# Optimization experiments

Hardware: AMD Instinct MI355X
Metric: run time of the kernel (lower is better)

Reference implementation:

```python
import jax, jax.numpy as jnp
import numpy as np
import math

B, S, D, H, DFF, NB = 16, 512, 512, 8, 2048, 2
DK = D // H
L = 3 * NB  # NB blocks_1 layers + 2*NB blocks_2 layers
NEG = -1e32
LN_EPS = 1e-5


def _layernorm(x, g, b):
    mu = jnp.mean(x, -1, keepdims=True)
    var = jnp.mean((x - mu) ** 2, -1, keepdims=True)
    return (x - mu) * jax.lax.rsqrt(var + LN_EPS) * g + b


def _attention(q, k, v, mask, gamma, zero_pad):
    # q,k,v: [B,H,S,DK]; mask: [S,S] bool; gamma: [H]
    scores = jnp.einsum('bhid,bhjd->bhij', q, k) / math.sqrt(DK)
    maskf = mask.astype(scores.dtype)
    # no-grad distance-decay block (torch.no_grad + .detach())
    p = jax.nn.softmax(jnp.where(mask, scores, NEG), axis=-1) * maskf
    distcum = jnp.cumsum(p, axis=-1)
    disttot = jnp.sum(p, axis=-1, keepdims=True)
    idx = jnp.arange(S, dtype=scores.dtype)
    pos = jnp.abs(idx[None, :] - idx[:, None])  # |i-j|, [S,S]
    dist = jnp.sqrt(jnp.clip((disttot - distcum) * pos, 0.0, None))
    dist = jax.lax.stop_gradient(dist)
    g = -jax.nn.softplus(gamma)[None, :, None, None]  # [1,H,1,1]
    total_effect = jnp.clip(jnp.exp(dist * g), 1e-5, 1e5)
    scores = jnp.where(mask, scores * total_effect, NEG)
    attn = jax.nn.softmax(scores, axis=-1)
    if zero_pad:
        attn = attn.at[:, :, 0, :].set(0.0)
    return jnp.einsum('bhij,bhjd->bhid', attn, v)


def _mha(q, k, v, mask, zero_pad, Wk, bk, Wv, bv, Wo, bo, gam):
    # kq_same=True: queries also use the k projection
    def proj(x, W, b):
        return (x @ W + b).reshape(B, S, H, DK).transpose(0, 2, 1, 3)
    qh = proj(q, Wk, bk)
    kh = proj(k, Wk, bk)
    vh = proj(v, Wv, bv)
    out = _attention(qh, kh, vh, mask, gam, zero_pad)
    out = out.transpose(0, 2, 1, 3).reshape(B, S, D)
    return out @ Wo + bo


def _layer(mask_flag, query, key_, values, apply_pos, p):
    (Wk, bk, Wv, bv, Wo, bo, gam, g1, bn1, W1, bf1, W2, bf2, g2, bn2) = p
    idx = jnp.arange(S)
    if mask_flag == 1:
        mask = idx[None, :] <= idx[:, None]  # peek current + past
    else:
        mask = idx[None, :] < idx[:, None]   # strictly past
    zero_pad = (mask_flag == 0)
    q2 = _mha(query, key_, values, mask, zero_pad, Wk, bk, Wv, bv, Wo, bo, gam)
    query = _layernorm(query + q2, g1, bn1)
    if apply_pos:
        q2 = jax.nn.relu(query @ W1 + bf1) @ W2 + bf2
        query = _layernorm(query + q2, g2, bn2)
    return query


def _forward(q_embed_data, qa_embed_data, pid_embed_data, params):
    # emb_type='qid' (no 'pdiff') -> pid_embed_data unused inside attention
    def pslice(l):
        return tuple(a[l] for a in params)
    y = qa_embed_data
    x = q_embed_data
    for l in range(NB):  # blocks_1: self-attn on y, mask=1
        y = _layer(1, y, y, y, True, pslice(l))
    for i in range(NB):  # blocks_2: alternating (mask=1, no FFN) / (mask=0, values=y)
        x = _layer(1, x, x, x, False, pslice(NB + 2 * i))
        x = _layer(0, x, x, y, True, pslice(NB + 2 * i + 1))
    return x, y


def setup_inputs() -> dict:
    key = jax.random.key(0)
    ks = jax.random.split(key, 10)
    sD = 1.0 / math.sqrt(D)
    sF = 1.0 / math.sqrt(DFF)
    f32 = jnp.float32
    return {
        'q_embed_data': jax.random.normal(ks[0], (B, S, D), f32),
        'qa_embed_data': jax.random.normal(ks[1], (B, S, D), f32),
        'pid_embed_data': jax.random.normal(ks[2], (B, S, D), f32),
        'Wk': jax.random.normal(ks[3], (L, D, D), f32) * sD,
        'bk': jnp.zeros((L, D), f32),
        'Wv': jax.random.normal(ks[4], (L, D, D), f32) * sD,
        'bv': jnp.zeros((L, D), f32),
        'Wo': jax.random.normal(ks[5], (L, D, D), f32) * sD,
        'bo': jnp.zeros((L, D), f32),
        'gammas': jax.random.normal(ks[6], (L, H), f32) * 0.5,
        'ln1_g': jnp.ones((L, D), f32),
        'ln1_b': jnp.zeros((L, D), f32),
        'W1': jax.random.normal(ks[7], (L, D, DFF), f32) * sD,
        'b1': jnp.zeros((L, DFF), f32),
        'W2': jax.random.normal(ks[8], (L, DFF, D), f32) * sF,
        'b2': jnp.zeros((L, D), f32),
        'ln2_g': jnp.ones((L, D), f32),
        'ln2_b': jnp.zeros((L, D), f32),
    }


def reference(q_embed_data, qa_embed_data, pid_embed_data, Wk, bk, Wv, bv, Wo, bo,
              gammas, ln1_g, ln1_b, W1, b1, W2, b2, ln2_g, ln2_b):
    params = (Wk, bk, Wv, bv, Wo, bo, gammas, ln1_g, ln1_b, W1, b1, W2, b2, ln2_g, ln2_b)
    x, y = _forward(q_embed_data, qa_embed_data, pid_embed_data, params)
    return (x, y)
```

## Files before the change

kernel.cpp:

```cpp
#include <hip/hip_runtime.h>
#include <hip/hip_bf16.h>

#define Bsz  16
#define Sl   512
#define Dm   512
#define Hn   8
#define DKh  64
#define DFFn 2048
#define MROWS (Bsz * Sl)
#define NEGV (-1e32f)

typedef _Float16 f16;
typedef f16 f16x8 __attribute__((ext_vector_type(8)));
typedef f16 f16x4 __attribute__((ext_vector_type(4)));
typedef float f32x4 __attribute__((ext_vector_type(4)));

#define GLDS16(g, l) __builtin_amdgcn_global_load_lds( \
    (const __attribute__((address_space(1))) void*)(g), \
    (__attribute__((address_space(3))) void*)(l), 16, 0, 0)

__global__ void k_copy2(const float* __restrict__ in, float* __restrict__ out,
                        f16* __restrict__ outh, int n) {
    int i = blockIdx.x * 256 + threadIdx.x;
    if (i < n) { float v = in[i]; out[i] = v; outh[i] = (f16)v; }
}

__global__ __launch_bounds__(256) void k_wconv(const float* __restrict__ src,
        f16* __restrict__ dst, int K, int N, int lmap)
{
    __shared__ float T[32][36];
    int z = blockIdx.z;
    int ls = lmap ? (z < 2 ? z : 2 * z - 1) : z;
    const float* S = src + (size_t)ls * K * N;
    f16* Dt = dst + (size_t)z * K * N;
    int n0 = blockIdx.x * 32, k0 = blockIdx.y * 32;
    int t = threadIdx.x;
    int r = t >> 3, c = (t & 7) * 4;
    float4 v = *(const float4*)(S + (size_t)(k0 + r) * N + n0 + c);
    T[r][c] = v.x; T[r][c + 1] = v.y; T[r][c + 2] = v.z; T[r][c + 3] = v.w;
    __syncthreads();
    int n = t >> 3, kq = (t & 7) * 4;
    f16x4 o = { (f16)T[kq][n], (f16)T[kq + 1][n], (f16)T[kq + 2][n], (f16)T[kq + 3][n] };
    *(f16x4*)(Dt + (size_t)(n0 + n) * K + k0 + kq) = o;
}

template <int RELU, int OUT16, int VTOUT, int BK64>
__global__ __launch_bounds__(256) void k_gemm(
    const f16* __restrict__ A, const f16* __restrict__ Bt,
    const float* __restrict__ bias, float* __restrict__ C, f16* __restrict__ Ch,
    int M, int N, int K)
{
    constexpr int HL = BK64 ? 2 : 1;
    constexpr int BUF = HL * 4096;
    __shared__ f16 As[2 * BUF];
    __shared__ f16 Bs[2 * BUF];
    int tid = threadIdx.x;
    int w = tid >> 6, lane = tid & 63;
    int ln = lane & 15, rg = lane >> 4;
    int wr = w >> 1, wc = w & 1;
    int m0 = blockIdx.y * 128, n0 = blockIdx.x * 128;

    int s0 = tid, s1 = 256 + tid;
    int r0s = s0 >> 2, c0s = ((s0 & 3) ^ ((s0 >> 3) & 3));
    int r1s = s1 >> 2, c1s = ((s1 & 3) ^ ((s1 >> 3) & 3));

    const f16* a0 = A + (size_t)(m0 + r0s) * K + c0s * 8;
    const f16* a1 = A + (size_t)(m0 + r1s) * K + c1s * 8;
    const f16* b0 = Bt + (size_t)(n0 + r0s) * K + c0s * 8;
    const f16* b1 = Bt + (size_t)(n0 + r1s) * K + c1s * 8;

    int cc8 = (rg ^ ((ln >> 1) & 3)) * 8;

    f32x4 acc[4][4] = {};

    int nk = K >> (BK64 ? 6 : 5);

    auto STAGE = [&](int nb, int kt) {
        f16* lA = As + nb * BUF + w * 512;
        f16* lB = Bs + nb * BUF + w * 512;
        GLDS16(a0 + kt, lA);
        GLDS16(a1 + kt, lA + 2048);
        GLDS16(b0 + kt, lB);
        GLDS16(b1 + kt, lB + 2048);
        if (BK64) {
            GLDS16(a0 + kt + 32, lA + 4096);
            GLDS16(a1 + kt + 32, lA + 4096 + 2048);
            GLDS16(b0 + kt + 32, lB + 4096);
            GLDS16(b1 + kt + 32, lB + 4096 + 2048);
        }
    };

    STAGE(0, 0);
    __syncthreads();

    int cur = 0;
    for (int t = 0; t < nk; ++t) {
        if (t + 1 < nk) STAGE(cur ^ 1, (t + 1) << (BK64 ? 6 : 5));

#pragma unroll
        for (int hh = 0; hh < HL; ++hh) {
            const f16* Ab = As + cur * BUF + hh * 4096;
            const f16* Bb = Bs + cur * BUF + hh * 4096;
            f16x8 af[4], bf[4];
#pragma unroll
            for (int i = 0; i < 4; ++i) {
                int m = wr * 64 + i * 16 + ln;
                af[i] = *(const f16x8*)(Ab + m * 32 + cc8);
                int nn = wc * 64 + i * 16 + ln;
                bf[i] = *(const f16x8*)(Bb + nn * 32 + cc8);
            }
#pragma unroll
            for (int i = 0; i < 4; ++i)
#pragma unroll
                for (int j = 0; j < 4; ++j)
                    acc[i][j] = __builtin_amdgcn_mfma_f32_16x16x32_f16(af[i], bf[j], acc[i][j], 0, 0, 0);
        }

        __syncthreads();
        cur ^= 1;
    }

#pragma unroll
    for (int j = 0; j < 4; ++j) {
        int col = n0 + wc * 64 + j * 16 + ln;
        float bj = bias[col];
#pragma unroll
        for (int i = 0; i < 4; ++i) {
            int rb = m0 + wr * 64 + i * 16 + rg * 4;
            if (VTOUT) {
                int bq = rb >> 9, s = rb & 511;
                int hh = col >> 6, dk = col & 63;
                f16x4 o;
#pragma unroll
                for (int r = 0; r < 4; ++r) o[r] = (f16)(acc[i][j][r] + bj);
                *(f16x4*)(Ch + (((size_t)(bq * 8 + hh) * 64 + dk) << 9) + s) = o;
            } else {
#pragma unroll
                for (int r = 0; r < 4; ++r) {
                    float v = acc[i][j][r] + bj;
                    if (RELU) v = fmaxf(v, 0.f);
                    if (OUT16) Ch[(size_t)(rb + r) * N + col] = (f16)v;
                    else       C [(size_t)(rb + r) * N + col] = v;
                }
            }
        }
    }
}

__global__ __launch_bounds__(256, 4) void k_attn(
    const f16* __restrict__ Qh, const f16* __restrict__ VT,
    f16* __restrict__ O, const float* __restrict__ gam, int maskflag)
{
    __shared__ float Sc[16][516];
    f16* Ph = (f16*)Sc;

    int tid = threadIdx.x;
    int w = tid >> 6, lane = tid & 63;
    int ln = lane & 15, rg = lane >> 4;

    int bid = blockIdx.x;
    int lbid = (bid & 7) * 512 + (bid >> 3);
    int tile = 31 - (lbid & 31);
    int bh = lbid >> 5;
    int b = bh >> 3, h = bh & 7;
    int i0 = tile * 16;
    int jtc = (tile >> 2) + 1;
    int units = jtc * 4;

    const f16* Qbase = Qh + ((size_t)b * Sl) * Dm + h * DKh;

    float gm = gam[h];
    float g = -((gm > 20.f) ? gm : log1pf(__expf(gm)));

    f16x8 aq0 = *(const f16x8*)(Qbase + (size_t)(i0 + ln) * Dm + rg * 8);
    f16x8 aq1 = *(const f16x8*)(Qbase + (size_t)(i0 + ln) * Dm + 32 + rg * 8);

    for (int u = w; u < units; u += 4) {
        const f16* kb = Qbase + (size_t)(u * 16 + ln) * Dm + rg * 8;
        f16x8 b0 = *(const f16x8*)(kb);
        f16x8 b1 = *(const f16x8*)(kb + 32);
        f32x4 c = {};
        c = __builtin_amdgcn_mfma_f32_16x16x32_f16(aq0, b0, c, 0, 0, 0);
        c = __builtin_amdgcn_mfma_f32_16x16x32_f16(aq1, b1, c, 0, 0, 0);
#pragma unroll
        for (int r = 0; r < 4; ++r)
            Sc[rg * 4 + r][u * 16 + ln] = c[r];
    }
    __syncthreads();

    int jbase = lane * jtc;
    float st[4][8];
    if ((jtc & 3) == 0) {
#pragma unroll
        for (int q = 0; q < 4; ++q) {
            int r = w * 4 + q;
            float4 t0 = *(float4*)&Sc[r][jbase];
            st[q][0] = t0.x; st[q][1] = t0.y; st[q][2] = t0.z; st[q][3] = t0.w;
            if (jtc == 8) {
                float4 t1 = *(float4*)&Sc[r][jbase + 4];
                st[q][4] = t1.x; st[q][5] = t1.y; st[q][6] = t1.z; st[q][7] = t1.w;
            }
        }
    } else {
#pragma unroll
        for (int q = 0; q < 4; ++q) {
            int r = w * 4 + q;
#pragma unroll
            for (int k = 0; k < 8; ++k)
                if (k < jtc) st[q][k] = Sc[r][jbase + k];
        }
    }
    __syncthreads();

    int im = i0 + w * 4;
    float cs[4][8], run[4], sl[4];
#pragma unroll
    for (int q = 0; q < 4; ++q) {
        int jmax = maskflag ? (im + q) : (im + q - 1);
        run[q] = 0.f;
#pragma unroll
        for (int k = 0; k < 8; ++k) if (k < jtc) {
            int j = jbase + k;
            float s = (j <= jmax) ? st[q][k] * 0.125f : NEGV;
            st[q][k] = s;
            run[q] += __expf(s);
            cs[q][k] = run[q];
        }
        sl[q] = run[q];
    }
#pragma unroll
    for (int off = 1; off < 64; off <<= 1) {
        float n0 = __shfl_up(sl[0], off);
        float n1 = __shfl_up(sl[1], off);
        float n2 = __shfl_up(sl[2], off);
        float n3 = __shfl_up(sl[3], off);
        if (lane >= off) { sl[0] += n0; sl[1] += n1; sl[2] += n2; sl[3] += n3; }
    }
    float Z2[4];
#pragma unroll
    for (int q = 0; q < 4; ++q) {
        float excl = sl[q] - run[q];
        float Z = __shfl(sl[q], 63);
        float inv = 1.f / Z;
        int i = im + q;
        int jmax = maskflag ? i : (i - 1);
        float z2 = 0.f;
#pragma unroll
        for (int k = 0; k < 8; ++k) if (k < jtc) {
            int j = jbase + k;
            float rem = (Z - excl - cs[q][k]) * inv;
            float pos = fabsf((float)(i - j));
            float dd = fmaxf(rem * pos, 0.f);
            float te = __expf(sqrtf(dd) * g);
            te = fminf(fmaxf(te, 1e-5f), 1e5f);
            float sc = (j <= jmax) ? st[q][k] * te : NEGV;
            float pe = __expf(sc);
            st[q][k] = pe;
            z2 += pe;
        }
        Z2[q] = z2;
    }
#pragma unroll
    for (int off = 32; off >= 1; off >>= 1) {
        Z2[0] += __shfl_xor(Z2[0], off);
        Z2[1] += __shfl_xor(Z2[1], off);
        Z2[2] += __shfl_xor(Z2[2], off);
        Z2[3] += __shfl_xor(Z2[3], off);
    }
#pragma unroll
    for (int q = 0; q < 4; ++q) {
        int r = w * 4 + q;
        int i = im + q;
        float inv2 = 1.f / Z2[q];
        int zp = (maskflag == 0) && (i == 0);
        if (jtc == 8) {
            int slot = (lane & ~7) | ((lane & 7) ^ (r & 7));
            f16x8 o8;
#pragma unroll
            for (int k = 0; k < 8; ++k)
                o8[k] = (f16)(zp ? 0.f : st[q][k] * inv2);
            *(f16x8*)(Ph + r * 512 + slot * 8) = o8;
        } else {
#pragma unroll
            for (int k = 0; k < 8; ++k) if (k < jtc) {
                int j = jbase + k;
                int cj = j >> 3;
                int slot = (cj & ~7) | ((cj & 7) ^ (r & 7));
                float a = zp ? 0.f : st[q][k] * inv2;
                Ph[r * 512 + slot * 8 + (j & 7)] = (f16)a;
            }
        }
    }
    __syncthreads();

    const f16* vbase = VT + ((size_t)bh * 64 + w * 16 + ln) * 512 + rg * 8;
    f32x4 oa0 = {}, oa1 = {};
#pragma unroll
    for (int f = 0; f < 16; ++f) if (f < 2 * jtc) {
        f16x8 bv = *(const f16x8*)(vbase + (f >> 1) * 64 + (f & 1) * 32);
        int c = (f >> 1) * 8 + (f & 1) * 4 + rg;
        int slot = (c & ~7) | ((c & 7) ^ (ln & 7));
        f16x8 ap = *(const f16x8*)(Ph + ln * 512 + slot * 8);
        if (f & 1) oa1 = __builtin_amdgcn_mfma_f32_16x16x32_f16(ap, bv, oa1, 0, 0, 0);
        else       oa0 = __builtin_amdgcn_mfma_f32_16x16x32_f16(ap, bv, oa0, 0, 0, 0);
    }
    f32x4 oa = oa0 + oa1;

    f16* ob = O + ((size_t)b * Sl + i0 + rg * 4) * Dm + h * DKh + w * 16 + ln;
#pragma unroll
    for (int r = 0; r < 4; ++r)
        ob[(size_t)r * Dm] = (f16)oa[r];
}

__global__ __launch_bounds__(256) void k_ln(
    const float* __restrict__ Xn, const float* __restrict__ Rr,
    const float* __restrict__ gw, const float* __restrict__ bw,
    float* __restrict__ Out, f16* __restrict__ Outh)
{
    int tid = threadIdx.x;
    int w = tid >> 6, lane = tid & 63;
    int row = blockIdx.x * 4 + w;
    const float* xr = Xn + (size_t)row * Dm;
    const float* rr = Rr + (size_t)row * Dm;
    int c0 = lane * 4, c1 = 256 + lane * 4;
    float4 va = *(const float4*)(xr + c0);
    float4 vb = *(const float4*)(xr + c1);
    float4 ra = *(const float4*)(rr + c0);
    float4 rb = *(const float4*)(rr + c1);
    va.x += ra.x; va.y += ra.y; va.z += ra.z; va.w += ra.w;
    vb.x += rb.x; vb.y += rb.y; vb.z += rb.z; vb.w += rb.w;
    float sum = va.x + va.y + va.z + va.w + vb.x + vb.y + vb.z + vb.w;
#pragma unroll
    for (int off = 32; off >= 1; off >>= 1) sum += __shfl_xor(sum, off);
    float mu = sum * (1.f / 512.f);
    float var = 0.f;
    {
        float d;
        d = va.x - mu; var += d * d;  d = va.y - mu; var += d * d;
        d = va.z - mu; var += d * d;  d = va.w - mu; var += d * d;
        d = vb.x - mu; var += d * d;  d = vb.y - mu; var += d * d;
        d = vb.z - mu; var += d * d;  d = vb.w - mu; var += d * d;
    }
#pragma unroll
    for (int off = 32; off >= 1; off >>= 1) var += __shfl_xor(var, off);
    float rs = rsqrtf(var * (1.f / 512.f) + 1e-5f);
    float4 ga = *(const float4*)(gw + c0);
    float4 gb = *(const float4*)(gw + c1);
    float4 ba = *(const float4*)(bw + c0);
    float4 bb = *(const float4*)(bw + c1);
    float4 oa, ob;
    oa.x = (va.x - mu) * rs * ga.x + ba.x;  oa.y = (va.y - mu) * rs * ga.y + ba.y;
    oa.z = (va.z - mu) * rs * ga.z + ba.z;  oa.w = (va.w - mu) * rs * ga.w + ba.w;
    ob.x = (vb.x - mu) * rs * gb.x + bb.x;  ob.y = (vb.y - mu) * rs * gb.y + bb.y;
    ob.z = (vb.z - mu) * rs * gb.z + bb.z;  ob.w = (vb.w - mu) * rs * gb.w + bb.w;
    float* orow = Out + (size_t)row * Dm;
    f16* ohrow = Outh + (size_t)row * Dm;
    *(float4*)(orow + c0) = oa;
    *(float4*)(orow + c1) = ob;
    f16x4 ha = { (f16)oa.x, (f16)oa.y, (f16)oa.z, (f16)oa.w };
    f16x4 hb = { (f16)ob.x, (f16)ob.y, (f16)ob.z, (f16)ob.w };
    *(f16x4*)(ohrow + c0) = ha;
    *(f16x4*)(ohrow + c1) = hb;
}

extern "C" void kernel_launch(void* const* d_in, const int* in_sizes, int n_in,
                              void* d_out, int out_size, void* d_ws, size_t ws_size,
                              hipStream_t stream)
{
    const float* q_emb  = (const float*)d_in[0];
    const float* qa_emb = (const float*)d_in[1];
    const float* Wk  = (const float*)d_in[3];
    const float* bk  = (const float*)d_in[4];
    const float* Wv  = (const float*)d_in[5];
    const float* bv  = (const float*)d_in[6];
    const float* Wo  = (const float*)d_in[7];
    const float* bo  = (const float*)d_in[8];
    const float* gam = (const float*)d_in[9];
    const float* l1g = (const float*)d_in[10];
    const float* l1b = (const float*)d_in[11];
    const float* W1  = (const float*)d_in[12];
    const float* b1  = (const float*)d_in[13];
    const float* W2  = (const float*)d_in[14];
    const float* b2  = (const float*)d_in[15];
    const float* l2g = (const float*)d_in[16];
    const float* l2b = (const float*)d_in[17];
    float* outp = (float*)d_out;

    const size_t NE  = (size_t)MROWS * Dm;
    const size_t WDD = (size_t)Dm * Dm;
    const size_t WDF = (size_t)Dm * DFFn;

    float* xbuf = (float*)d_ws;
    float* ybuf = xbuf + NE;
    float* t2   = ybuf + NE;
    f16* xh  = (f16*)(t2 + NE);
    f16* yh  = xh + NE;
    f16* R   = yh + NE;
    f16* qh  = R;
    f16* vt  = R + 2 * NE;
    f16* t1h = R + 3 * NE;
    f16* fbh = R;
    f16* wkh = R + 4 * NE;
    f16* wvh = wkh + 6 * WDD;
    f16* woh = wvh + 6 * WDD;
    f16* w1h = woh + 6 * WDD;
    f16* w2h = w1h + 4 * WDF;

    k_wconv<<<dim3(Dm / 32, Dm / 32, 6), 256, 0, stream>>>(Wk, wkh, Dm, Dm, 0);
    k_wconv<<<dim3(Dm / 32, Dm / 32, 6), 256, 0, stream>>>(Wv, wvh, Dm, Dm, 0);
    k_wconv<<<dim3(Dm / 32, Dm / 32, 6), 256, 0, stream>>>(Wo, woh, Dm, Dm, 0);
    k_wconv<<<dim3(DFFn / 32, Dm / 32, 4), 256, 0, stream>>>(W1, w1h, Dm, DFFn, 1);
    k_wconv<<<dim3(Dm / 32, DFFn / 32, 4), 256, 0, stream>>>(W2, w2h, DFFn, Dm, 1);

    const int n = (int)NE;
    k_copy2<<<n / 256, 256, 0, stream>>>(q_emb,  xbuf, xh, n);
    k_copy2<<<n / 256, 256, 0, stream>>>(qa_emb, ybuf, yh, n);

    auto gemm16 = [&](const f16* A, const f16* Bt, const float* bias, f16* C,
                      int M, int N, int K) {
        k_gemm<0, 1, 0, 1><<<dim3(N / 128, M / 128), 256, 0, stream>>>(A, Bt, bias, nullptr, C, M, N, K);
    };
    auto gemm32 = [&](const f16* A, const f16* Bt, const float* bias, float* C,
                      int M, int N, int K) {
        k_gemm<0, 0, 0, 1><<<dim3(N / 128, M / 128), 256, 0, stream>>>(A, Bt, bias, C, nullptr, M, N, K);
    };
    auto gemmvt = [&](const f16* A, const f16* Bt, const float* bias, f16* C) {
        k_gemm<0, 1, 1, 1><<<dim3(Dm / 128, MROWS / 128), 256, 0, stream>>>(A, Bt, bias, nullptr, C, MROWS, Dm, Dm);
    };

    auto layer = [&](int l, int maskflag, float* Xq, f16* Xqh, f16* Xvh,
                     bool apply_pos, float* finalOut) {
        gemm16(Xqh, wkh + (size_t)l * WDD, bk + l * Dm, qh, MROWS, Dm, Dm);
        gemmvt(Xvh, wvh + (size_t)l * WDD, bv + l * Dm, vt);
        k_attn<<<Bsz * Hn * 32, 256, 0, stream>>>(qh, vt, t1h, gam + l * Hn, maskflag);
        gemm32(t1h, woh + (size_t)l * WDD, bo + l * Dm, t2, MROWS, Dm, Dm);
        if (apply_pos) {
            k_ln<<<MROWS / 4, 256, 0, stream>>>(t2, Xq, l1g + l * Dm, l1b + l * Dm, Xq, Xqh);
            int sl = (l < 2) ? l : ((l + 1) >> 1);
            k_gemm<1, 1, 0, 0><<<dim3(DFFn / 128, MROWS / 128), 256, 0, stream>>>(
                Xqh, w1h + (size_t)sl * WDF, b1 + l * DFFn, nullptr, fbh, MROWS, DFFn, Dm);
            k_gemm<0, 0, 0, 1><<<dim3(Dm / 128, MROWS / 128), 256, 0, stream>>>(
                fbh, w2h + (size_t)sl * WDF, b2 + l * Dm, t2, nullptr, MROWS, Dm, DFFn);
            k_ln<<<MROWS / 4, 256, 0, stream>>>(t2, Xq, l2g + l * Dm, l2b + l * Dm,
                                                finalOut ? finalOut : Xq, Xqh);
        } else {
            k_ln<<<MROWS / 4, 256, 0, stream>>>(t2, Xq, l1g + l * Dm, l1b + l * Dm,
                                                finalOut ? finalOut : Xq, Xqh);
        }
    };

    const size_t NEo = NE;
    layer(0, 1, ybuf, yh, yh, true, nullptr);
    layer(1, 1, ybuf, yh, yh, true, outp + NEo);
    layer(2, 1, xbuf, xh, xh, false, nullptr);
    layer(3, 0, xbuf, xh, yh, true, nullptr);
    layer(4, 1, xbuf, xh, xh, false, nullptr);
    layer(5, 0, xbuf, xh, yh, true, outp);
}
```

Baseline: 1.186 ms.

## Fuse K and V projections into one GEMM and template attention on tile count

When the query and value inputs are the same tensor, the K and V projection weights are packed side by side and run as a single GEMM with N=1024. The epilogue writes the first half row-major and the second half transposed for V, and a small kernel concatenates the two bias vectors. The attention kernel is also templated on the number of key tiles, so its loops fully unroll without runtime guards. The recomputation pass now rereads scores from LDS instead of keeping the cumulative sums in registers. This trades fewer launches and better GEMM occupancy against eight instantiated code paths and extra LDS reads.

```diff
diff --git a/kernel.cpp b/kernel.cpp
--- a/kernel.cpp
+++ b/kernel.cpp
@@ -25,14 +25,21 @@
     if (i < n) { float v = in[i]; out[i] = v; outh[i] = (f16)v; }
 }
 
+__global__ void k_bcat(const float* __restrict__ bk, const float* __restrict__ bv,
+                       float* __restrict__ bkv) {
+    int i = blockIdx.x * 256 + threadIdx.x;
+    int z = i >> 10, c = i & 1023;
+    bkv[i] = (c < 512) ? bk[z * 512 + c] : bv[z * 512 + c - 512];
+}
+
 __global__ __launch_bounds__(256) void k_wconv(const float* __restrict__ src,
-        f16* __restrict__ dst, int K, int N, int lmap)
+        f16* __restrict__ dst, int K, int N, int lmap, size_t zstride)
 {
     __shared__ float T[32][36];
     int z = blockIdx.z;
     int ls = lmap ? (z < 2 ? z : 2 * z - 1) : z;
     const float* S = src + (size_t)ls * K * N;
-    f16* Dt = dst + (size_t)z * K * N;
+    f16* Dt = dst + (size_t)z * zstride;
     int n0 = blockIdx.x * 32, k0 = blockIdx.y * 32;
     int t = threadIdx.x;
     int r = t >> 3, c = (t & 7) * 4;
@@ -127,13 +134,28 @@
 #pragma unroll
         for (int i = 0; i < 4; ++i) {
             int rb = m0 + wr * 64 + i * 16 + rg * 4;
-            if (VTOUT) {
+            if (VTOUT == 1) {
                 int bq = rb >> 9, s = rb & 511;
                 int hh = col >> 6, dk = col & 63;
                 f16x4 o;
 #pragma unroll
                 for (int r = 0; r < 4; ++r) o[r] = (f16)(acc[i][j][r] + bj);
                 *(f16x4*)(Ch + (((size_t)(bq * 8 + hh) * 64 + dk) << 9) + s) = o;
+            } else if (VTOUT == 2) {
+                if (n0 < 512) {
+#pragma unroll
+                    for (int r = 0; r < 4; ++r)
+                        Ch[(size_t)(rb + r) * 512 + col] = (f16)(acc[i][j][r] + bj);
+                } else {
+                    f16* Cv = (f16*)C;
+                    int colv = col - 512;
+                    int bq = rb >> 9, s = rb & 511;
+                    int hh = colv >> 6, dk = colv & 63;
+                    f16x4 o;
+#pragma unroll
+                    for (int r = 0; r < 4; ++r) o[r] = (f16)(acc[i][j][r] + bj);
+                    *(f16x4*)(Cv + (((size_t)(bq * 8 + hh) * 64 + dk) << 9) + s) = o;
+                }
             } else {
 #pragma unroll
                 for (int r = 0; r < 4; ++r) {
@@ -147,6 +169,139 @@
     }
 }
 
+template <int JTC>
+__device__ __forceinline__ void attn_body(
+    float (*Sc)[516], f16* Ph, const f16* Qbase, const f16* vbase, f16* ob,
+    f16x8 aq0, f16x8 aq1, float g,
+    int w, int lane, int ln, int rg, int i0, int maskflag)
+{
+#pragma unroll
+    for (int ui = 0; ui < JTC; ++ui) {
+        int u = w + ui * 4;
+        const f16* kb = Qbase + (size_t)(u * 16 + ln) * Dm + rg * 8;
+        f16x8 b0 = *(const f16x8*)(kb);
+        f16x8 b1 = *(const f16x8*)(kb + 32);
+        f32x4 c = {};
+        c = __builtin_amdgcn_mfma_f32_16x16x32_f16(aq0, b0, c, 0, 0, 0);
+        c = __builtin_amdgcn_mfma_f32_16x16x32_f16(aq1, b1, c, 0, 0, 0);
+#pragma unroll
+        for (int r = 0; r < 4; ++r)
+            Sc[rg * 4 + r][u * 16 + ln] = c[r];
+    }
+    __syncthreads();
+
+    int jbase = lane * JTC;
+    int im = i0 + w * 4;
+
+    float run[4];
+#pragma unroll
+    for (int q = 0; q < 4; ++q) {
+        int jmax = maskflag ? (im + q) : (im + q - 1);
+        float acc = 0.f;
+#pragma unroll
+        for (int k = 0; k < JTC; ++k) {
+            int j = jbase + k;
+            float s = (j <= jmax) ? Sc[w * 4 + q][j] * 0.125f : NEGV;
+            acc += __expf(s);
+        }
+        run[q] = acc;
+    }
+    float sl[4] = { run[0], run[1], run[2], run[3] };
+#pragma unroll
+    for (int off = 1; off < 64; off <<= 1) {
+        float n0 = __shfl_up(sl[0], off);
+        float n1 = __shfl_up(sl[1], off);
+        float n2 = __shfl_up(sl[2], off);
+        float n3 = __shfl_up(sl[3], off);
+        if (lane >= off) { sl[0] += n0; sl[1] += n1; sl[2] += n2; sl[3] += n3; }
+    }
+
+    float pe2s[4][JTC];
+    float Z2[4];
+#pragma unroll
+    for (int q = 0; q < 4; ++q) {
+        float excl = sl[q] - run[q];
+        float Z = __shfl(sl[q], 63);
+        float inv = 1.f / Z;
+        int i = im + q;
+        int jmax = maskflag ? i : (i - 1);
+        float csum = 0.f, z2 = 0.f;
+#pragma unroll
+        for (int k = 0; k < JTC; ++k) {
+            int j = jbase + k;
+            float s = (j <= jmax) ? Sc[w * 4 + q][j] * 0.125f : NEGV;
+            float pe = __expf(s);
+            csum += pe;
+            float rem = (Z - excl - csum) * inv;
+            float pos = fabsf((float)(i - j));
+            float dd = fmaxf(rem * pos, 0.f);
+            float te = __expf(sqrtf(dd) * g);
+            te = fminf(fmaxf(te, 1e-5f), 1e5f);
+            float sc = (j <= jmax) ? s * te : NEGV;
+            float pe2 = __expf(sc);
+            pe2s[q][k] = pe2;
+            z2 += pe2;
+        }
+        Z2[q] = z2;
+    }
+#pragma unroll
+    for (int off = 32; off >= 1; off >>= 1) {
+        Z2[0] += __shfl_xor(Z2[0], off);
+        Z2[1] += __shfl_xor(Z2[1], off);
+        Z2[2] += __shfl_xor(Z2[2], off);
+        Z2[3] += __shfl_xor(Z2[3], off);
+    }
+    __syncthreads();
+
+#pragma unroll
+    for (int q = 0; q < 4; ++q) {
+        int r = w * 4 + q;
+        float inv2 = 1.f / Z2[q];
+        int zp = (maskflag == 0) && (im + q == 0);
+        if constexpr (JTC == 8) {
+            int slot = (lane & ~7) | ((lane & 7) ^ (r & 7));
+            f16x8 o8;
+#pragma unroll
+            for (int k = 0; k < 8; ++k)
+                o8[k] = (f16)(zp ? 0.f : pe2s[q][k] * inv2);
+            *(f16x8*)(Ph + r * 512 + slot * 8) = o8;
+        } else if constexpr (JTC == 4) {
+            int cj = lane >> 1;
+            int slot = (cj & ~7) | ((cj & 7) ^ (r & 7));
+            f16x4 o4;
+#pragma unroll
+            for (int k = 0; k < 4; ++k)
+                o4[k] = (f16)(zp ? 0.f : pe2s[q][k] * inv2);
+            *(f16x4*)(Ph + r * 512 + slot * 8 + (lane & 1) * 4) = o4;
+        } else {
+#pragma unroll
+            for (int k = 0; k < JTC; ++k) {
+                int j = jbase + k;
+                int cj = j >> 3;
+                int slot = (cj & ~7) | ((cj & 7) ^ (r & 7));
+                Ph[r * 512 + slot * 8 + (j & 7)] =
+                    (f16)(zp ? 0.f : pe2s[q][k] * inv2);
+            }
+        }
+    }
+    __syncthreads();
+
+    f32x4 oa0 = {}, oa1 = {};
+#pragma unroll
+    for (int f = 0; f < 2 * JTC; ++f) {
+        f16x8 bv = *(const f16x8*)(vbase + (f >> 1) * 64 + (f & 1) * 32);
+        int c = (f >> 1) * 8 + (f & 1) * 4 + rg;
+        int slot = (c & ~7) | ((c & 7) ^ (ln & 7));
+        f16x8 ap = *(const f16x8*)(Ph + ln * 512 + slot * 8);
+        if (f & 1) oa1 = __builtin_amdgcn_mfma_f32_16x16x32_f16(ap, bv, oa1, 0, 0, 0);
+        else       oa0 = __builtin_amdgcn_mfma_f32_16x16x32_f16(ap, bv, oa0, 0, 0, 0);
+    }
+    f32x4 oa = oa0 + oa1;
+#pragma unroll
+    for (int r = 0; r < 4; ++r)
+        ob[(size_t)r * Dm] = (f16)oa[r];
+}
+
 __global__ __launch_bounds__(256, 4) void k_attn(
     const f16* __restrict__ Qh, const f16* __restrict__ VT,
     f16* __restrict__ O, const float* __restrict__ gam, int maskflag)
@@ -165,9 +320,10 @@
     int b = bh >> 3, h = bh & 7;
     int i0 = tile * 16;
     int jtc = (tile >> 2) + 1;
-    int units = jtc * 4;
 
     const f16* Qbase = Qh + ((size_t)b * Sl) * Dm + h * DKh;
+    const f16* vbase = VT + ((size_t)bh * 64 + w * 16 + ln) * 512 + rg * 8;
+    f16* ob = O + ((size_t)b * Sl + i0 + rg * 4) * Dm + h * DKh + w * 16 + ln;
 
     float gm = gam[h];
     float g = -((gm > 20.f) ? gm : log1pf(__expf(gm)));
@@ -175,141 +331,16 @@
     f16x8 aq0 = *(const f16x8*)(Qbase + (size_t)(i0 + ln) * Dm + rg * 8);
     f16x8 aq1 = *(const f16x8*)(Qbase + (size_t)(i0 + ln) * Dm + 32 + rg * 8);
 
-    for (int u = w; u < units; u += 4) {
-        const f16* kb = Qbase + (size_t)(u * 16 + ln) * Dm + rg * 8;
-        f16x8 b0 = *(const f16x8*)(kb);
-        f16x8 b1 = *(const f16x8*)(kb + 32);
-        f32x4 c = {};
-        c = __builtin_amdgcn_mfma_f32_16x16x32_f16(aq0, b0, c, 0, 0, 0);
-        c = __builtin_amdgcn_mfma_f32_16x16x32_f16(aq1, b1, c, 0, 0, 0);
-#pragma unroll
-        for (int r = 0; r < 4; ++r)
-            Sc[rg * 4 + r][u * 16 + ln] = c[r];
-    }
-    __syncthreads();
-
-    int jbase = lane * jtc;
-    float st[4][8];
-    if ((jtc & 3) == 0) {
-#pragma unroll
-        for (int q = 0; q < 4; ++q) {
-            int r = w * 4 + q;
-            float4 t0 = *(float4*)&Sc[r][jbase];
-            st[q][0] = t0.x; st[q][1] = t0.y; st[q][2] = t0.z; st[q][3] = t0.w;
-            if (jtc == 8) {
-                float4 t1 = *(float4*)&Sc[r][jbase + 4];
-                st[q][4] = t1.x; st[q][5] = t1.y; st[q][6] = t1.z; st[q][7] = t1.w;
-            }
-        }
-    } else {
-#pragma unroll
-        for (int q = 0; q < 4; ++q) {
-            int r = w * 4 + q;
-#pragma unroll
-            for (int k = 0; k < 8; ++k)
-                if (k < jtc) st[q][k] = Sc[r][jbase + k];
-        }
-    }
-    __syncthreads();
-
-    int im = i0 + w * 4;
-    float cs[4][8], run[4], sl[4];
-#pragma unroll
-    for (int q = 0; q < 4; ++q) {
-        int jmax = maskflag ? (im + q) : (im + q - 1);
-        run[q] = 0.f;
-#pragma unroll
-        for (int k = 0; k < 8; ++k) if (k < jtc) {
-            int j = jbase + k;
-            float s = (j <= jmax) ? st[q][k] * 0.125f : NEGV;
-            st[q][k] = s;
-            run[q] += __expf(s);
-            cs[q][k] = run[q];
-        }
-        sl[q] = run[q];
-    }
-#pragma unroll
-    for (int off = 1; off < 64; off <<= 1) {
-        float n0 = __shfl_up(sl[0], off);
-        float n1 = __shfl_up(sl[1], off);
-        float n2 = __shfl_up(sl[2], off);
-        float n3 = __shfl_up(sl[3], off);
-        if (lane >= off) { sl[0] += n0; sl[1] += n1; sl[2] += n2; sl[3] += n3; }
-    }
-    float Z2[4];
-#pragma unroll
-    for (int q = 0; q < 4; ++q) {
-        float excl = sl[q] - run[q];
-        float Z = __shfl(sl[q], 63);
-        float inv = 1.f / Z;
-        int i = im + q;
-        int jmax = maskflag ? i : (i - 1);
-        float z2 = 0.f;
-#pragma unroll
-        for (int k = 0; k < 8; ++k) if (k < jtc) {
-            int j = jbase + k;
-            float rem = (Z - excl - cs[q][k]) * inv;
-            float pos = fabsf((float)(i - j));
-            float dd = fmaxf(rem * pos, 0.f);
-            float te = __expf(sqrtf(dd) * g);
-            te = fminf(fmaxf(te, 1e-5f), 1e5f);
-            float sc = (j <= jmax) ? st[q][k] * te : NEGV;
-            float pe = __expf(sc);
-            st[q][k] = pe;
-            z2 += pe;
-        }
-        Z2[q] = z2;
-    }
-#pragma unroll
-    for (int off = 32; off >= 1; off >>= 1) {
-        Z2[0] += __shfl_xor(Z2[0], off);
-        Z2[1] += __shfl_xor(Z2[1], off);
-        Z2[2] += __shfl_xor(Z2[2], off);
-        Z2[3] += __shfl_xor(Z2[3], off);
-    }
-#pragma unroll
-    for (int q = 0; q < 4; ++q) {
-        int r = w * 4 + q;
-        int i = im + q;
-        float inv2 = 1.f / Z2[q];
-        int zp = (maskflag == 0) && (i == 0);
-        if (jtc == 8) {
-            int slot = (lane & ~7) | ((lane & 7) ^ (r & 7));
-            f16x8 o8;
-#pragma unroll
-            for (int k = 0; k < 8; ++k)
-                o8[k] = (f16)(zp ? 0.f : st[q][k] * inv2);
-            *(f16x8*)(Ph + r * 512 + slot * 8) = o8;
-        } else {
-#pragma unroll
-            for (int k = 0; k < 8; ++k) if (k < jtc) {
-                int j = jbase + k;
-                int cj = j >> 3;
-                int slot = (cj & ~7) | ((cj & 7) ^ (r & 7));
-                float a = zp ? 0.f : st[q][k] * inv2;
-                Ph[r * 512 + slot * 8 + (j & 7)] = (f16)a;
-            }
-        }
-    }
-    __syncthreads();
-
-    const f16* vbase = VT + ((size_t)bh * 64 + w * 16 + ln) * 512 + rg * 8;
-    f32x4 oa0 = {}, oa1 = {};
-#pragma unroll
-    for (int f = 0; f < 16; ++f) if (f < 2 * jtc) {
-        f16x8 bv = *(const f16x8*)(vbase + (f >> 1) * 64 + (f & 1) * 32);
-        int c = (f >> 1) * 8 + (f & 1) * 4 + rg;
-        int slot = (c & ~7) | ((c & 7) ^ (ln & 7));
-        f16x8 ap = *(const f16x8*)(Ph + ln * 512 + slot * 8);
-        if (f & 1) oa1 = __builtin_amdgcn_mfma_f32_16x16x32_f16(ap, bv, oa1, 0, 0, 0);
-        else       oa0 = __builtin_amdgcn_mfma_f32_16x16x32_f16(ap, bv, oa0, 0, 0, 0);
-    }
-    f32x4 oa = oa0 + oa1;
-
-    f16* ob = O + ((size_t)b * Sl + i0 + rg * 4) * Dm + h * DKh + w * 16 + ln;
-#pragma unroll
-    for (int r = 0; r < 4; ++r)
-        ob[(size_t)r * Dm] = (f16)oa[r];
+    switch (jtc) {
+    case 1: attn_body<1>(Sc, Ph, Qbase, vbase, ob, aq0, aq1, g, w, lane, ln, rg, i0, maskflag); break;
+    case 2: attn_body<2>(Sc, Ph, Qbase, vbase, ob, aq0, aq1, g, w, lane, ln, rg, i0, maskflag); break;
+    case 3: attn_body<3>(Sc, Ph, Qbase, vbase, ob, aq0, aq1, g, w, lane, ln, rg, i0, maskflag); break;
+    case 4: attn_body<4>(Sc, Ph, Qbase, vbase, ob, aq0, aq1, g, w, lane, ln, rg, i0, maskflag); break;
+    case 5: attn_body<5>(Sc, Ph, Qbase, vbase, ob, aq0, aq1, g, w, lane, ln, rg, i0, maskflag); break;
+    case 6: attn_body<6>(Sc, Ph, Qbase, vbase, ob, aq0, aq1, g, w, lane, ln, rg, i0, maskflag); break;
+    case 7: attn_body<7>(Sc, Ph, Qbase, vbase, ob, aq0, aq1, g, w, lane, ln, rg, i0, maskflag); break;
+    default: attn_body<8>(Sc, Ph, Qbase, vbase, ob, aq0, aq1, g, w, lane, ln, rg, i0, maskflag); break;
+    }
 }
 
 __global__ __launch_bounds__(256) void k_ln(
@@ -389,6 +420,7 @@
     const size_t NE  = (size_t)MROWS * Dm;
     const size_t WDD = (size_t)Dm * Dm;
     const size_t WDF = (size_t)Dm * DFFn;
+    const size_t WKV = 2 * WDD;
 
     float* xbuf = (float*)d_ws;
     float* ybuf = xbuf + NE;
@@ -400,38 +432,39 @@
     f16* vt  = R + 2 * NE;
     f16* t1h = R + 3 * NE;
     f16* fbh = R;
-    f16* wkh = R + 4 * NE;
-    f16* wvh = wkh + 6 * WDD;
-    f16* woh = wvh + 6 * WDD;
+    f16* wkvh = R + 4 * NE;
+    f16* woh = wkvh + 6 * WKV;
     f16* w1h = woh + 6 * WDD;
     f16* w2h = w1h + 4 * WDF;
-
-    k_wconv<<<dim3(Dm / 32, Dm / 32, 6), 256, 0, stream>>>(Wk, wkh, Dm, Dm, 0);
-    k_wconv<<<dim3(Dm / 32, Dm / 32, 6), 256, 0, stream>>>(Wv, wvh, Dm, Dm, 0);
-    k_wconv<<<dim3(Dm / 32, Dm / 32, 6), 256, 0, stream>>>(Wo, woh, Dm, Dm, 0);
-    k_wconv<<<dim3(DFFn / 32, Dm / 32, 4), 256, 0, stream>>>(W1, w1h, Dm, DFFn, 1);
-    k_wconv<<<dim3(Dm / 32, DFFn / 32, 4), 256, 0, stream>>>(W2, w2h, DFFn, Dm, 1);
+    float* bkv = (float*)(w2h + 4 * WDF);
+
+    k_wconv<<<dim3(Dm / 32, Dm / 32, 6), 256, 0, stream>>>(Wk, wkvh, Dm, Dm, 0, WKV);
+    k_wconv<<<dim3(Dm / 32, Dm / 32, 6), 256, 0, stream>>>(Wv, wkvh + WDD, Dm, Dm, 0, WKV);
+    k_wconv<<<dim3(Dm / 32, Dm / 32, 6), 256, 0, stream>>>(Wo, woh, Dm, Dm, 0, WDD);
+    k_wconv<<<dim3(DFFn / 32, Dm / 32, 4), 256, 0, stream>>>(W1, w1h, Dm, DFFn, 1, WDF);
+    k_wconv<<<dim3(Dm / 32, DFFn / 32, 4), 256, 0, stream>>>(W2, w2h, DFFn, Dm, 1, WDF);
+    k_bcat<<<24, 256, 0, stream>>>(bk, bv, bkv);
 
     const int n = (int)NE;
     k_copy2<<<n / 256, 256, 0, stream>>>(q_emb,  xbuf, xh, n);
     k_copy2<<<n / 256, 256, 0, stream>>>(qa_emb, ybuf, yh, n);
 
-    auto gemm16 = [&](const f16* A, const f16* Bt, const float* bias, f16* C,
-                      int M, int N, int K) {
-        k_gemm<0, 1, 0, 1><<<dim3(N / 128, M / 128), 256, 0, stream>>>(A, Bt, bias, nullptr, C, M, N, K);
-    };
     auto gemm32 = [&](const f16* A, const f16* Bt, const float* bias, float* C,
                       int M, int N, int K) {
         k_gemm<0, 0, 0, 1><<<dim3(N / 128, M / 128), 256, 0, stream>>>(A, Bt, bias, C, nullptr, M, N, K);
     };
-    auto gemmvt = [&](const f16* A, const f16* Bt, const float* bias, f16* C) {
-        k_gemm<0, 1, 1, 1><<<dim3(Dm / 128, MROWS / 128), 256, 0, stream>>>(A, Bt, bias, nullptr, C, MROWS, Dm, Dm);
-    };
 
     auto layer = [&](int l, int maskflag, float* Xq, f16* Xqh, f16* Xvh,
                      bool apply_pos, float* finalOut) {
-        gemm16(Xqh, wkh + (size_t)l * WDD, bk + l * Dm, qh, MROWS, Dm, Dm);
-        gemmvt(Xvh, wvh + (size_t)l * WDD, bv + l * Dm, vt);
+        if (Xqh == Xvh) {
+            k_gemm<0, 1, 2, 1><<<dim3(1024 / 128, MROWS / 128), 256, 0, stream>>>(
+                Xqh, wkvh + (size_t)l * WKV, bkv + l * 1024, (float*)vt, qh, MROWS, 1024, Dm);
+        } else {
+            k_gemm<0, 1, 0, 1><<<dim3(Dm / 128, MROWS / 128), 256, 0, stream>>>(
+                Xqh, wkvh + (size_t)l * WKV, bk + l * Dm, nullptr, qh, MROWS, Dm, Dm);
+            k_gemm<0, 1, 1, 1><<<dim3(Dm / 128, MROWS / 128), 256, 0, stream>>>(
+                Xvh, wkvh + (size_t)l * WKV + WDD, bv + l * Dm, nullptr, vt, MROWS, Dm, Dm);
+        }
         k_attn<<<Bsz * Hn * 32, 256, 0, stream>>>(qh, vt, t1h, gam + l * Hn, maskflag);
         gemm32(t1h, woh + (size_t)l * WDD, bo + l * Dm, t2, MROWS, Dm, Dm);
         if (apply_pos) {
```

Result: faster. 1.136 ms (-4.2%).
